# Kernel optimization log

Hardware: AMD Instinct MI355X
Metric: run time of the kernel (lower is better)

The kernel has to match this reference:

```python
import jax, jax.numpy as jnp
import numpy as np

N_CLS = 8192
FEAT_DIM = 512
BATCH = 1024
PROTO_M = 0.95
TEMPERATURE = 0.1
BASE_TEMPERATURE = 0.1
EPS = 1e-12  # F.normalize eps


def setup_inputs() -> dict:
    key = jax.random.key(0)
    k1, k2, k3 = jax.random.split(key, 3)
    features = jax.random.normal(k1, (BATCH, FEAT_DIM), dtype=jnp.float32)
    features = features / jnp.maximum(jnp.linalg.norm(features, axis=1, keepdims=True), EPS)
    labels = jax.random.randint(k2, (BATCH,), 0, N_CLS, dtype=jnp.int64 if jax.config.jax_enable_x64 else jnp.int32)
    prototypes = jax.random.normal(k3, (N_CLS, FEAT_DIM), dtype=jnp.float32)
    prototypes = prototypes / jnp.maximum(jnp.linalg.norm(prototypes, axis=1, keepdims=True), EPS)
    return {"features": features, "labels": labels, "prototypes": prototypes}


def _l2norm_vec(v):
    # F.normalize(v, dim=0) for a 1-D vector
    return v / jnp.maximum(jnp.linalg.norm(v), EPS)


def reference(features, labels, prototypes):
    # --- sequential per-sample EMA prototype update (order matters) ---
    def step(protos, fl):
        f, l = fl
        new_p = _l2norm_vec(protos[l] * PROTO_M + f * (1.0 - PROTO_M))
        return protos.at[l].set(new_p), None

    protos, _ = jax.lax.scan(step, prototypes, (features, labels))

    # --- dispersion loss over prototype pairs ---
    logits = (protos @ protos.T) / TEMPERATURE            # [n_cls, n_cls]
    n = protos.shape[0]
    mask = 1.0 - jnp.eye(n, dtype=logits.dtype)           # off-diagonal pairs
    # log of mean exp over negatives (exactly the original, non-stabilized, form;
    # prototypes are unit-norm so |logits| <= 1/T and exp is safe)
    mean_prob_neg = jnp.log((mask * jnp.exp(logits)).sum(axis=1) / mask.sum(axis=1))
    # original drops NaN rows; with n_cls > 1 mask.sum(1) == n_cls-1 > 0 so none occur
    loss = (TEMPERATURE / BASE_TEMPERATURE) * mean_prob_neg.mean()
    return loss
```

## Files before the change

### kernel.cpp

```cpp
#include <hip/hip_runtime.h>
#include <hip/hip_fp8.h>
#include <stdint.h>

#define N_CLS 8192
#define FEAT  512
#define BATCH 1024
#define NTI   32
#define NTJ   64
#define NBLK  1056
#define NSLOT 8
#define SLOTB 24576

typedef __attribute__((ext_vector_type(4))) float f32x4;
typedef __attribute__((ext_vector_type(2))) long longx2;

__device__ inline unsigned char f2fp8(float x) {
    __hip_fp8_e4m3 q(x);
    return q.__x;
}

__global__ __launch_bounds__(256) void ema_kernel(
    const float* __restrict__ features, const int* __restrict__ labels,
    const float* __restrict__ protos,
    unsigned char* __restrict__ Phi8, float* __restrict__ rowsum) {
    const int row  = blockIdx.x * 4 + (threadIdx.x >> 6);
    const int lane = threadIdx.x & 63;
    if (lane == 0) rowsum[row] = 0.f;

    float p[8];
    #pragma unroll
    for (int j = 0; j < 8; ++j) p[j] = protos[(size_t)row * FEAT + j * 64 + lane];

    for (int c = 0; c < BATCH / 64; ++c) {
        int lab = labels[c * 64 + lane];
        unsigned long long m = __ballot(lab == row);
        while (m) {
            int b = __builtin_ctzll(m);
            m &= m - 1;
            int s = c * 64 + b;
            float ss = 0.f;
            #pragma unroll
            for (int j = 0; j < 8; ++j) {
                float f = features[(size_t)s * FEAT + j * 64 + lane];
                p[j] = p[j] * 0.95f + f * 0.05f;
                ss += p[j] * p[j];
            }
            #pragma unroll
            for (int off = 32; off; off >>= 1) ss += __shfl_xor(ss, off);
            float inv = 1.0f / fmaxf(sqrtf(ss), 1e-12f);
            #pragma unroll
            for (int j = 0; j < 8; ++j) p[j] *= inv;
        }
    }
    #pragma unroll
    for (int j = 0; j < 8; ++j)
        Phi8[(size_t)row * FEAT + j * 64 + lane] = f2fp8(p[j]);
}

__global__ __launch_bounds__(512, 4) void gemm_disp_kernel(
    const unsigned char* __restrict__ Phi8, float* __restrict__ rowsum) {
    __shared__ __align__(16) char smem[3 * SLOTB];

    int bid = blockIdx.x;
    int u = (bid & 7) * (NBLK / 8) + (bid >> 3);
    int i = 0;
    while (u >= NTJ - 2 * i) { u -= NTJ - 2 * i; ++i; }
    const int j = 2 * i + u;
    const bool diagovl = ((j >> 1) == i);

    const int w    = threadIdx.x >> 6;
    const int lane = threadIdx.x & 63;
    const int wr = w >> 1, wc = w & 1;
    const int h = lane >> 4;
    const int r = lane & 15;
    const int rseg = (h ^ ((r >> 1) & 3)) * 16;

    const int Ibase = i * 256, Jbase = j * 128;

    f32x4 acc[4][4];
    #pragma unroll
    for (int m = 0; m < 4; ++m)
        #pragma unroll
        for (int n = 0; n < 4; ++n) acc[m][n] = (f32x4){0.f, 0.f, 0.f, 0.f};

    const int srow = lane >> 2;
    const int sseg = (lane & 3) ^ ((lane >> 3) & 3);
    const unsigned char* gA =
        Phi8 + (size_t)(Ibase + w * 32 + srow) * FEAT + sseg * 16;
    const unsigned char* gB =
        Phi8 + (size_t)(Jbase + w * 16 + srow) * FEAT + sseg * 16;

#define STAGE(s)                                                              \
    {                                                                         \
        char* base = smem + ((s) % 3) * SLOTB;                                \
        __builtin_amdgcn_global_load_lds(                                     \
            (const __attribute__((address_space(1))) void*)(gA + (s) * 64),   \
            (__attribute__((address_space(3))) void*)(base + w * 2048),       \
            16, 0, 0);                                                        \
        __builtin_amdgcn_global_load_lds(                                     \
            (const __attribute__((address_space(1))) void*)(gA + 16 * FEAT + (s) * 64), \
            (__attribute__((address_space(3))) void*)(base + w * 2048 + 1024),\
            16, 0, 0);                                                        \
        __builtin_amdgcn_global_load_lds(                                     \
            (const __attribute__((address_space(1))) void*)(gB + (s) * 64),   \
            (__attribute__((address_space(3))) void*)(base + 16384 + w * 1024),\
            16, 0, 0);                                                        \
    }

#define MF8(ai, bi, mi, ni)                                                   \
    acc[mi][ni] = __builtin_amdgcn_mfma_f32_16x16x32_fp8_fp8(                 \
        ai[0], bi[0], acc[mi][ni], 0, 0, 0);                                  \
    acc[mi][ni] = __builtin_amdgcn_mfma_f32_16x16x32_fp8_fp8(                 \
        ai[1], bi[1], acc[mi][ni], 0, 0, 0);

#define SLOT(s, TAIL)                                                         \
    {                                                                         \
        const char* As = smem + ((s) % 3) * SLOTB;                            \
        const char* Bs = As + 16384;                                          \
        longx2 a0, a1, a2, a3, b0, b1, b2, b3;                                \
        b0 = *(const longx2*)(Bs + (wc * 64 +  0 + r) * 64 + rseg);           \
        b1 = *(const longx2*)(Bs + (wc * 64 + 16 + r) * 64 + rseg);           \
        b2 = *(const longx2*)(Bs + (wc * 64 + 32 + r) * 64 + rseg);           \
        b3 = *(const longx2*)(Bs + (wc * 64 + 48 + r) * 64 + rseg);           \
        a0 = *(const longx2*)(As + (wr * 64 +  0 + r) * 64 + rseg);           \
        a1 = *(const longx2*)(As + (wr * 64 + 16 + r) * 64 + rseg);           \
        a2 = *(const longx2*)(As + (wr * 64 + 32 + r) * 64 + rseg);           \
        a3 = *(const longx2*)(As + (wr * 64 + 48 + r) * 64 + rseg);           \
        __builtin_amdgcn_s_setprio(1);                                        \
        MF8(a0, b0, 0, 0) MF8(a1, b0, 1, 0) MF8(a2, b0, 2, 0) MF8(a3, b0, 3, 0) \
        MF8(a0, b1, 0, 1) MF8(a1, b1, 1, 1) MF8(a2, b1, 2, 1) MF8(a3, b1, 3, 1) \
        MF8(a0, b2, 0, 2) MF8(a1, b2, 1, 2) MF8(a2, b2, 2, 2) MF8(a3, b2, 3, 2) \
        MF8(a0, b3, 0, 3) MF8(a1, b3, 1, 3) MF8(a2, b3, 2, 3) MF8(a3, b3, 3, 3) \
        __builtin_amdgcn_s_setprio(0);                                        \
        TAIL                                                                  \
    }

#define TAIL_MID(s)                                                           \
    STAGE((s) + 2)                                                            \
    asm volatile("s_waitcnt vmcnt(3)" ::: "memory");                          \
    __builtin_amdgcn_s_barrier();
#define TAIL_6                                                                \
    asm volatile("s_waitcnt vmcnt(0)" ::: "memory");                          \
    __builtin_amdgcn_s_barrier();
#define TAIL_7

    STAGE(0) STAGE(1)
    asm volatile("s_waitcnt vmcnt(3)" ::: "memory");
    __builtin_amdgcn_s_barrier();

    SLOT(0, TAIL_MID(0)) SLOT(1, TAIL_MID(1)) SLOT(2, TAIL_MID(2))
    SLOT(3, TAIL_MID(3)) SLOT(4, TAIL_MID(4)) SLOT(5, TAIL_MID(5))
    SLOT(6, TAIL_6)
    SLOT(7, TAIL_7)

    #pragma unroll
    for (int m = 0; m < 4; ++m)
        #pragma unroll
        for (int n = 0; n < 4; ++n)
            #pragma unroll
            for (int q = 0; q < 4; ++q) {
                float v = __expf(acc[m][n][q] * 10.0f);
                if (diagovl &&
                    (Ibase + wr * 64 + m * 16 + h * 4 + q) ==
                    (Jbase + wc * 64 + n * 16 + r))
                    v = 0.f;
                acc[m][n][q] = v;
            }

    #pragma unroll
    for (int m = 0; m < 4; ++m) {
        float rs[4];
        #pragma unroll
        for (int q = 0; q < 4; ++q)
            rs[q] = acc[m][0][q] + acc[m][1][q] + acc[m][2][q] + acc[m][3][q];
        #pragma unroll
        for (int q = 0; q < 4; ++q)
            #pragma unroll
            for (int off = 1; off < 16; off <<= 1) rs[q] += __shfl_xor(rs[q], off);
        if (r == 0) {
            #pragma unroll
            for (int q = 0; q < 4; ++q)
                atomicAdd(&rowsum[Ibase + wr * 64 + m * 16 + h * 4 + q], rs[q]);
        }
    }

    if (!diagovl) {
        #pragma unroll
        for (int n = 0; n < 4; ++n) {
            float cs = 0.f;
            #pragma unroll
            for (int m = 0; m < 4; ++m)
                #pragma unroll
                for (int q = 0; q < 4; ++q) cs += acc[m][n][q];
            cs += __shfl_xor(cs, 16);
            cs += __shfl_xor(cs, 32);
            if (lane < 16)
                atomicAdd(&rowsum[Jbase + wc * 64 + n * 16 + r], cs);
        }
    }
}

__global__ __launch_bounds__(512) void loss_kernel(
    const float* __restrict__ rowsum, float* __restrict__ out) {
    __shared__ float red[8];
    float s = 0.f;
    for (int i = threadIdx.x; i < N_CLS; i += 512)
        s += logf(rowsum[i] * (1.0f / (float)(N_CLS - 1)));
    #pragma unroll
    for (int off = 32; off; off >>= 1) s += __shfl_xor(s, off);
    if ((threadIdx.x & 63) == 0) red[threadIdx.x >> 6] = s;
    __syncthreads();
    if (threadIdx.x == 0) {
        float tot = 0.f;
        #pragma unroll
        for (int i = 0; i < 8; ++i) tot += red[i];
        out[0] = tot * (1.0f / (float)N_CLS);
    }
}

extern "C" void kernel_launch(void* const* d_in, const int* in_sizes, int n_in,
                              void* d_out, int out_size, void* d_ws, size_t ws_size,
                              hipStream_t stream) {
    (void)in_sizes; (void)n_in; (void)out_size; (void)ws_size;
    const float* features = (const float*)d_in[0];
    const int*   labels   = (const int*)d_in[1];
    const float* protos   = (const float*)d_in[2];
    float* out = (float*)d_out;

    unsigned char* Phi8 = (unsigned char*)d_ws;
    float* rowsum = (float*)(Phi8 + (size_t)N_CLS * FEAT);

    ema_kernel<<<N_CLS / 4, 256, 0, stream>>>(features, labels, protos, Phi8, rowsum);
    gemm_disp_kernel<<<NBLK, 512, 0, stream>>>(Phi8, rowsum);
    loss_kernel<<<1, 512, 0, stream>>>(rowsum, out);
}
```

Measured before the change: 58.83 us.

## Shrink GEMM tile to 256x64 with 128-byte K slices and double buffering

Changes the symmetric prototype Gram tile from 256x128 to 256x64, doubling the block count to 2112. Each K stage now loads 128 bytes instead of 64, giving 4 stages instead of 8, with a new XOR swizzle over 8 segments. The pipeline moves from three LDS buffers with a lookahead of two to double buffering with one stage of prefetch. The aim is more parallelism and fewer barriers per block. The cost is more redundant A loads, more atomics, less data reuse per block and weaker latency hiding.

```diff
diff --git a/kernel.cpp b/kernel.cpp
--- a/kernel.cpp
+++ b/kernel.cpp
@@ -6,10 +6,10 @@
 #define FEAT  512
 #define BATCH 1024
 #define NTI   32
-#define NTJ   64
-#define NBLK  1056
-#define NSLOT 8
-#define SLOTB 24576
+#define NTJ   128
+#define NBLK  2112
+#define NSLOT 4
+#define SLOTB 40960
 
 typedef __attribute__((ext_vector_type(4))) float f32x4;
 typedef __attribute__((ext_vector_type(2))) long longx2;
@@ -59,110 +59,116 @@
 
 __global__ __launch_bounds__(512, 4) void gemm_disp_kernel(
     const unsigned char* __restrict__ Phi8, float* __restrict__ rowsum) {
-    __shared__ __align__(16) char smem[3 * SLOTB];
+    __shared__ __align__(16) char smem[2 * SLOTB];
 
     int bid = blockIdx.x;
     int u = (bid & 7) * (NBLK / 8) + (bid >> 3);
     int i = 0;
-    while (u >= NTJ - 2 * i) { u -= NTJ - 2 * i; ++i; }
-    const int j = 2 * i + u;
-    const bool diagovl = ((j >> 1) == i);
+    while (u >= NTJ - 4 * i) { u -= NTJ - 4 * i; ++i; }
+    const int j = 4 * i + u;
+    const bool diagovl = ((j >> 2) == i);
 
     const int w    = threadIdx.x >> 6;
     const int lane = threadIdx.x & 63;
     const int wr = w >> 1, wc = w & 1;
     const int h = lane >> 4;
     const int r = lane & 15;
-    const int rseg = (h ^ ((r >> 1) & 3)) * 16;
-
-    const int Ibase = i * 256, Jbase = j * 128;
-
-    f32x4 acc[4][4];
+    const int xr = ((r >> 1) & 3) | ((r & 1) << 2);
+    const int s0 = (h ^ (xr & 3)) | (xr & 4);
+
+    const int Ibase = i * 256, Jbase = j * 64;
+
+    f32x4 acc[4][2];
     #pragma unroll
     for (int m = 0; m < 4; ++m)
         #pragma unroll
-        for (int n = 0; n < 4; ++n) acc[m][n] = (f32x4){0.f, 0.f, 0.f, 0.f};
-
-    const int srow = lane >> 2;
-    const int sseg = (lane & 3) ^ ((lane >> 3) & 3);
+        for (int n = 0; n < 2; ++n) acc[m][n] = (f32x4){0.f, 0.f, 0.f, 0.f};
+
+    const int srr  = lane >> 3;
+    const int sseg = (lane & 7) ^ (((srr >> 1) & 3) | ((srr & 1) << 2));
     const unsigned char* gA =
-        Phi8 + (size_t)(Ibase + w * 32 + srow) * FEAT + sseg * 16;
+        Phi8 + (size_t)(Ibase + w * 32 + srr) * FEAT + sseg * 16;
     const unsigned char* gB =
-        Phi8 + (size_t)(Jbase + w * 16 + srow) * FEAT + sseg * 16;
+        Phi8 + (size_t)(Jbase + w * 8 + srr) * FEAT + sseg * 16;
 
 #define STAGE(s)                                                              \
     {                                                                         \
-        char* base = smem + ((s) % 3) * SLOTB;                                \
+        char* base = smem + ((s) & 1) * SLOTB;                                \
+        _Pragma("unroll")                                                     \
+        for (int c = 0; c < 4; ++c) {                                         \
+            __builtin_amdgcn_global_load_lds(                                 \
+                (const __attribute__((address_space(1))) void*)                \
+                    (gA + (size_t)(c * 8) * FEAT + (s) * 128),                \
+                (__attribute__((address_space(3))) void*)                     \
+                    (base + w * 4096 + c * 1024), 16, 0, 0);                  \
+        }                                                                     \
         __builtin_amdgcn_global_load_lds(                                     \
-            (const __attribute__((address_space(1))) void*)(gA + (s) * 64),   \
-            (__attribute__((address_space(3))) void*)(base + w * 2048),       \
-            16, 0, 0);                                                        \
-        __builtin_amdgcn_global_load_lds(                                     \
-            (const __attribute__((address_space(1))) void*)(gA + 16 * FEAT + (s) * 64), \
-            (__attribute__((address_space(3))) void*)(base + w * 2048 + 1024),\
-            16, 0, 0);                                                        \
-        __builtin_amdgcn_global_load_lds(                                     \
-            (const __attribute__((address_space(1))) void*)(gB + (s) * 64),   \
-            (__attribute__((address_space(3))) void*)(base + 16384 + w * 1024),\
-            16, 0, 0);                                                        \
-    }
-
-#define MF8(ai, bi, mi, ni)                                                   \
+            (const __attribute__((address_space(1))) void*)(gB + (s) * 128),  \
+            (__attribute__((address_space(3))) void*)                         \
+                (base + 32768 + w * 1024), 16, 0, 0);                         \
+    }
+
+#define MFT(av, bv, mi, ni)                                                   \
     acc[mi][ni] = __builtin_amdgcn_mfma_f32_16x16x32_fp8_fp8(                 \
-        ai[0], bi[0], acc[mi][ni], 0, 0, 0);                                  \
+        av[0], bv[0], acc[mi][ni], 0, 0, 0);                                  \
     acc[mi][ni] = __builtin_amdgcn_mfma_f32_16x16x32_fp8_fp8(                 \
-        ai[1], bi[1], acc[mi][ni], 0, 0, 0);
-
-#define SLOT(s, TAIL)                                                         \
+        av[1], bv[1], acc[mi][ni], 0, 0, 0);
+
+#define SLOT(s, DO_STAGE, TAIL)                                               \
     {                                                                         \
-        const char* As = smem + ((s) % 3) * SLOTB;                            \
-        const char* Bs = As + 16384;                                          \
-        longx2 a0, a1, a2, a3, b0, b1, b2, b3;                                \
-        b0 = *(const longx2*)(Bs + (wc * 64 +  0 + r) * 64 + rseg);           \
-        b1 = *(const longx2*)(Bs + (wc * 64 + 16 + r) * 64 + rseg);           \
-        b2 = *(const longx2*)(Bs + (wc * 64 + 32 + r) * 64 + rseg);           \
-        b3 = *(const longx2*)(Bs + (wc * 64 + 48 + r) * 64 + rseg);           \
-        a0 = *(const longx2*)(As + (wr * 64 +  0 + r) * 64 + rseg);           \
-        a1 = *(const longx2*)(As + (wr * 64 + 16 + r) * 64 + rseg);           \
-        a2 = *(const longx2*)(As + (wr * 64 + 32 + r) * 64 + rseg);           \
-        a3 = *(const longx2*)(As + (wr * 64 + 48 + r) * 64 + rseg);           \
+        const char* As = smem + ((s) & 1) * SLOTB;                            \
+        const char* Bs = As + 32768;                                          \
+        if (DO_STAGE) STAGE((s) + 1)                                          \
+        longx2 aL0, aL1, aL2, aL3, aH0, aH1, aH2, aH3, bL0, bL1, bH0, bH1;    \
+        bL0 = *(const longx2*)(Bs + (wc * 32 +  0 + r) * 128 + s0 * 16);      \
+        bH0 = *(const longx2*)(Bs + (wc * 32 +  0 + r) * 128 + (s0 ^ 4) * 16);\
+        bL1 = *(const longx2*)(Bs + (wc * 32 + 16 + r) * 128 + s0 * 16);      \
+        bH1 = *(const longx2*)(Bs + (wc * 32 + 16 + r) * 128 + (s0 ^ 4) * 16);\
+        aL0 = *(const longx2*)(As + (wr * 64 +  0 + r) * 128 + s0 * 16);      \
+        aH0 = *(const longx2*)(As + (wr * 64 +  0 + r) * 128 + (s0 ^ 4) * 16);\
+        aL1 = *(const longx2*)(As + (wr * 64 + 16 + r) * 128 + s0 * 16);      \
+        aH1 = *(const longx2*)(As + (wr * 64 + 16 + r) * 128 + (s0 ^ 4) * 16);\
+        aL2 = *(const longx2*)(As + (wr * 64 + 32 + r) * 128 + s0 * 16);      \
+        aH2 = *(const longx2*)(As + (wr * 64 + 32 + r) * 128 + (s0 ^ 4) * 16);\
+        aL3 = *(const longx2*)(As + (wr * 64 + 48 + r) * 128 + s0 * 16);      \
+        aH3 = *(const longx2*)(As + (wr * 64 + 48 + r) * 128 + (s0 ^ 4) * 16);\
         __builtin_amdgcn_s_setprio(1);                                        \
-        MF8(a0, b0, 0, 0) MF8(a1, b0, 1, 0) MF8(a2, b0, 2, 0) MF8(a3, b0, 3, 0) \
-        MF8(a0, b1, 0, 1) MF8(a1, b1, 1, 1) MF8(a2, b1, 2, 1) MF8(a3, b1, 3, 1) \
-        MF8(a0, b2, 0, 2) MF8(a1, b2, 1, 2) MF8(a2, b2, 2, 2) MF8(a3, b2, 3, 2) \
-        MF8(a0, b3, 0, 3) MF8(a1, b3, 1, 3) MF8(a2, b3, 2, 3) MF8(a3, b3, 3, 3) \
+        MFT(aL0, bL0, 0, 0) MFT(aL1, bL0, 1, 0) MFT(aL2, bL0, 2, 0)           \
+        MFT(aL3, bL0, 3, 0)                                                   \
+        MFT(aL0, bL1, 0, 1) MFT(aL1, bL1, 1, 1) MFT(aL2, bL1, 2, 1)           \
+        MFT(aL3, bL1, 3, 1)                                                   \
+        MFT(aH0, bH0, 0, 0) MFT(aH1, bH0, 1, 0) MFT(aH2, bH0, 2, 0)           \
+        MFT(aH3, bH0, 3, 0)                                                   \
+        MFT(aH0, bH1, 0, 1) MFT(aH1, bH1, 1, 1) MFT(aH2, bH1, 2, 1)           \
+        MFT(aH3, bH1, 3, 1)                                                   \
         __builtin_amdgcn_s_setprio(0);                                        \
         TAIL                                                                  \
     }
 
-#define TAIL_MID(s)                                                           \
-    STAGE((s) + 2)                                                            \
-    asm volatile("s_waitcnt vmcnt(3)" ::: "memory");                          \
-    __builtin_amdgcn_s_barrier();
-#define TAIL_6                                                                \
+#define TAIL_SYNC                                                             \
     asm volatile("s_waitcnt vmcnt(0)" ::: "memory");                          \
     __builtin_amdgcn_s_barrier();
-#define TAIL_7
-
-    STAGE(0) STAGE(1)
-    asm volatile("s_waitcnt vmcnt(3)" ::: "memory");
+#define TAIL_NONE
+
+    STAGE(0)
+    asm volatile("s_waitcnt vmcnt(0)" ::: "memory");
     __builtin_amdgcn_s_barrier();
 
-    SLOT(0, TAIL_MID(0)) SLOT(1, TAIL_MID(1)) SLOT(2, TAIL_MID(2))
-    SLOT(3, TAIL_MID(3)) SLOT(4, TAIL_MID(4)) SLOT(5, TAIL_MID(5))
-    SLOT(6, TAIL_6)
-    SLOT(7, TAIL_7)
+    SLOT(0, 1, TAIL_SYNC)
+    SLOT(1, 1, TAIL_SYNC)
+    SLOT(2, 1, TAIL_SYNC)
+    SLOT(3, 0, TAIL_NONE)
 
     #pragma unroll
     for (int m = 0; m < 4; ++m)
         #pragma unroll
-        for (int n = 0; n < 4; ++n)
+        for (int n = 0; n < 2; ++n)
             #pragma unroll
             for (int q = 0; q < 4; ++q) {
                 float v = __expf(acc[m][n][q] * 10.0f);
                 if (diagovl &&
                     (Ibase + wr * 64 + m * 16 + h * 4 + q) ==
-                    (Jbase + wc * 64 + n * 16 + r))
+                    (Jbase + wc * 32 + n * 16 + r))
                     v = 0.f;
                 acc[m][n][q] = v;
             }
@@ -172,7 +178,7 @@
         float rs[4];
         #pragma unroll
         for (int q = 0; q < 4; ++q)
-            rs[q] = acc[m][0][q] + acc[m][1][q] + acc[m][2][q] + acc[m][3][q];
+            rs[q] = acc[m][0][q] + acc[m][1][q];
         #pragma unroll
         for (int q = 0; q < 4; ++q)
             #pragma unroll
@@ -186,7 +192,7 @@
 
     if (!diagovl) {
         #pragma unroll
-        for (int n = 0; n < 4; ++n) {
+        for (int n = 0; n < 2; ++n) {
             float cs = 0.f;
             #pragma unroll
             for (int m = 0; m < 4; ++m)
@@ -195,7 +201,7 @@
             cs += __shfl_xor(cs, 16);
             cs += __shfl_xor(cs, 32);
             if (lane < 16)
-                atomicAdd(&rowsum[Jbase + wc * 64 + n * 16 + r], cs);
+                atomicAdd(&rowsum[Jbase + wc * 32 + n * 16 + r], cs);
         }
     }
 }
```

Result: slower. 83.29 us (+41.6%).
